# Kernel optimization log

Measured on AMD Instinct MI355X. Metric: run time of the kernel, lower is better.

Reference implementation:

```python
import jax, jax.numpy as jnp
import numpy as np

PROP_TIME = 8  # matches init_kwargs prop_time


def _patches(x, dil):
    # x: [B,1,H,W] -> [B,9,H,W]; 'same' padding with the given dilation,
    # matching torch.nn.functional.unfold(kernel_size=3, dilation=dil, padding=dil).
    return jax.lax.conv_general_dilated_patches(
        x,
        filter_shape=(3, 3),
        window_strides=(1, 1),
        padding=[(dil, dil), (dil, dil)],
        rhs_dilation=(dil, dil),
    )


def setup_inputs() -> dict:
    key = jax.random.key(0)
    k1, k2, k3, k4 = jax.random.split(key, 4)
    B, H, W = 4, 352, 1216
    guided1 = jax.random.normal(k1, (B, 9, H, W), dtype=jnp.float32)
    guided2 = jax.random.normal(k2, (B, 9, H, W), dtype=jnp.float32)
    fuse = jax.random.uniform(k3, (B, 2, H, W), dtype=jnp.float32)
    x = jax.random.normal(k4, (B, 1, H, W), dtype=jnp.float32)
    return {"guided1": guided1, "guided2": guided2, "fuse": fuse, "x": x}


def reference(guided1, guided2, fuse, x):
    # softmax over the 9 kernel taps -> spatially varying normalized kernels
    kern1 = jax.nn.softmax(guided1, axis=1)  # [B,9,H,W]
    kern2 = jax.nn.softmax(guided2, axis=1)  # [B,9,H,W]
    f1 = fuse[:, 0:1]  # [B,1,H,W]
    f2 = fuse[:, 1:2]
    for _ in range(PROP_TIME):
        p1 = _patches(x, 1)  # [B,9,H,W]
        p2 = _patches(x, 2)
        o1 = jnp.sum(p1 * kern1, axis=1, keepdims=True)  # [B,1,H,W]
        o2 = jnp.sum(p2 * kern2, axis=1, keepdims=True)
        x = o1 * f1 + o2 * f2
    return x
```

## Files before the change

kernel.cpp:

```cpp
#include <hip/hip_runtime.h>

#define HH 352
#define WW 1216
#define NB 4
#define HWSZ (HH * WW)
#define WQ 304
#define NQ (NB * HH * WQ)

typedef _Float16 half8 __attribute__((ext_vector_type(8)));


__global__ __launch_bounds__(256, 2) void softmax_premul_kernel(
    const float* __restrict__ g1, const float* __restrict__ g2,
    const float* __restrict__ fuse, _Float16* __restrict__ ko) {
    int q = blockIdx.x * 256 + threadIdx.x;
    if (q >= NQ) return;
    int b   = q / (HH * WQ);
    int rem = q - b * (HH * WQ);
    long gbase = (long)b * 9 * HWSZ + (long)rem * 4;
    long fbase = (long)b * 2 * HWSZ + (long)rem * 4;

    float4 t[18];
#pragma unroll
    for (int k = 0; k < 9; k++) t[k]     = *(const float4*)(g1 + gbase + (long)k * HWSZ);
#pragma unroll
    for (int k = 0; k < 9; k++) t[9 + k] = *(const float4*)(g2 + gbase + (long)k * HWSZ);
    float4 f1 = *(const float4*)(fuse + fbase);
    float4 f2 = *(const float4*)(fuse + fbase + HWSZ);

    float s1[4] = {0.f, 0.f, 0.f, 0.f}, s2[4] = {0.f, 0.f, 0.f, 0.f};
#pragma unroll
    for (int k = 0; k < 9; k++) {
        t[k].x = __expf(t[k].x); s1[0] += t[k].x;
        t[k].y = __expf(t[k].y); s1[1] += t[k].y;
        t[k].z = __expf(t[k].z); s1[2] += t[k].z;
        t[k].w = __expf(t[k].w); s1[3] += t[k].w;
    }
#pragma unroll
    for (int k = 9; k < 18; k++) {
        t[k].x = __expf(t[k].x); s2[0] += t[k].x;
        t[k].y = __expf(t[k].y); s2[1] += t[k].y;
        t[k].z = __expf(t[k].z); s2[2] += t[k].z;
        t[k].w = __expf(t[k].w); s2[3] += t[k].w;
    }
    float r1[4], r2[4];
    r1[0] = f1.x / s1[0]; r1[1] = f1.y / s1[1]; r1[2] = f1.z / s1[2]; r1[3] = f1.w / s1[3];
    r2[0] = f2.x / s2[0]; r2[1] = f2.y / s2[1]; r2[2] = f2.z / s2[2]; r2[3] = f2.w / s2[3];

    long obase = ((long)b * 9 * HWSZ + (long)rem * 4) * 2;
#pragma unroll
    for (int k = 0; k < 9; k++) {
        half8 o;
        o[0] = (_Float16)(t[k].x * r1[0]); o[1] = (_Float16)(t[9 + k].x * r2[0]);
        o[2] = (_Float16)(t[k].y * r1[1]); o[3] = (_Float16)(t[9 + k].y * r2[1]);
        o[4] = (_Float16)(t[k].z * r1[2]); o[5] = (_Float16)(t[9 + k].z * r2[2]);
        o[6] = (_Float16)(t[k].w * r1[3]); o[7] = (_Float16)(t[9 + k].w * r2[3]);
        *(half8*)(ko + obase + (long)k * HWSZ * 2) = o;
    }
}

#define CTH 8
#define CTQ 76
#define R1H 12
#define R1Q 78
#define X0H 16
#define X0Q 80
#define NREG (R1H * R1Q)

__global__ __launch_bounds__(512, 2) void prop2_kernel(
    const _Float16* __restrict__ kk,
    const float* __restrict__ xin, float* __restrict__ xout) {
    __shared__ float x0s[X0H][X0Q * 4];
    __shared__ float x1s[R1H][R1Q * 4];

    int tid  = threadIdx.x;
    int bidx = blockIdx.x;
    int tX = bidx & 3;
    int rr = bidx >> 2;
    int tY = rr % 44;
    int b  = rr / 44;
    int q0 = tX * CTQ;
    int h0 = tY * CTH;
    const float* xb = xin + (long)b * HWSZ;

    half8 kv[2][9];
    int own_r[2], own_c[2];
    bool own_v[2];
#pragma unroll
    for (int o = 0; o < 2; o++) {
        int idx = tid + o * 512;
        bool active = idx < NREG;
        int r = idx / R1Q;
        int c = idx - r * R1Q;
        own_r[o] = r; own_c[o] = c;
        int h  = h0 - 2 + r;
        int qg = q0 - 1 + c;
        bool valid = active && (h >= 0) && (h < HH) && (qg >= 0) && (qg < WQ);
        own_v[o] = active;
        long kb = ((long)b * 9 * HWSZ + (long)h * WW + qg * 4) * 2;
#pragma unroll
        for (int k = 0; k < 9; k++) {
            half8 z = {};
            kv[o][k] = valid ? *(const half8*)(kk + kb + (long)k * HWSZ * 2) : z;
        }
    }

    for (int i = tid; i < X0H * X0Q; i += 512) {
        int r = i / X0Q;
        int c = i - r * X0Q;
        int h  = h0 - 4 + r;
        int qg = q0 - 2 + c;
        float4 v = make_float4(0.f, 0.f, 0.f, 0.f);
        if (h >= 0 && h < HH && qg >= 0 && qg < WQ)
            v = *(const float4*)(xb + (long)h * WW + qg * 4);
        *(float4*)&x0s[r][c * 4] = v;
    }
    __syncthreads();

#pragma unroll
    for (int o = 0; o < 2; o++) {
        if (!own_v[o]) continue;
        int r = own_r[o], c = own_c[o];
        float rb[5][8];
#pragma unroll
        for (int y = 0; y < 5; y++) {
            const float* p = &x0s[r + y][4 * c + 2];
            float2 a = *(const float2*)(p);
            float4 m = *(const float4*)(p + 2);
            float2 z = *(const float2*)(p + 6);
            rb[y][0] = a.x; rb[y][1] = a.y;
            rb[y][2] = m.x; rb[y][3] = m.y; rb[y][4] = m.z; rb[y][5] = m.w;
            rb[y][6] = z.x; rb[y][7] = z.y;
        }
        float ov[4] = {0.f, 0.f, 0.f, 0.f};
#pragma unroll
        for (int ky = 0; ky < 3; ky++)
#pragma unroll
            for (int kx = 0; kx < 3; kx++) {
                int k = ky * 3 + kx;
#pragma unroll
                for (int j = 0; j < 4; j++) {
                    ov[j] = fmaf((float)kv[o][k][2 * j],     rb[ky + 1][j + 1 + kx], ov[j]);
                    ov[j] = fmaf((float)kv[o][k][2 * j + 1], rb[2 * ky][j + 2 * kx], ov[j]);
                }
            }
        *(float4*)&x1s[r][c * 4] = make_float4(ov[0], ov[1], ov[2], ov[3]);
    }
    __syncthreads();

#pragma unroll
    for (int o = 0; o < 2; o++) {
        int r = own_r[o], c = own_c[o];
        if (!own_v[o] || r < 2 || r >= 10 || c < 1 || c >= 77) continue;
        float rb[5][8];
#pragma unroll
        for (int y = 0; y < 5; y++) {
            const float* p = &x1s[r - 2 + y][4 * c - 2];
            float2 a = *(const float2*)(p);
            float4 m = *(const float4*)(p + 2);
            float2 z = *(const float2*)(p + 6);
            rb[y][0] = a.x; rb[y][1] = a.y;
            rb[y][2] = m.x; rb[y][3] = m.y; rb[y][4] = m.z; rb[y][5] = m.w;
            rb[y][6] = z.x; rb[y][7] = z.y;
        }
        float ov[4] = {0.f, 0.f, 0.f, 0.f};
#pragma unroll
        for (int ky = 0; ky < 3; ky++)
#pragma unroll
            for (int kx = 0; kx < 3; kx++) {
                int k = ky * 3 + kx;
#pragma unroll
                for (int j = 0; j < 4; j++) {
                    ov[j] = fmaf((float)kv[o][k][2 * j],     rb[ky + 1][j + 1 + kx], ov[j]);
                    ov[j] = fmaf((float)kv[o][k][2 * j + 1], rb[2 * ky][j + 2 * kx], ov[j]);
                }
            }
        int h  = h0 - 2 + r;
        int qg = q0 - 1 + c;
        *(float4*)(xout + (long)b * HWSZ + (long)h * WW + qg * 4) =
            make_float4(ov[0], ov[1], ov[2], ov[3]);
    }
}

extern "C" void kernel_launch(void* const* d_in, const int* in_sizes, int n_in,
                              void* d_out, int out_size, void* d_ws, size_t ws_size,
                              hipStream_t stream) {
    const float* g1   = (const float*)d_in[0];
    const float* g2   = (const float*)d_in[1];
    const float* fuse = (const float*)d_in[2];
    const float* x    = (const float*)d_in[3];
    float* out = (float*)d_out;

    _Float16* kk = (_Float16*)d_ws;
    float* bufA  = (float*)(kk + (size_t)NB * 9 * HWSZ * 2);

    int sm_blocks = (NQ + 255) / 256;
    softmax_premul_kernel<<<sm_blocks, 256, 0, stream>>>(g1, g2, fuse, kk);

    int pr_blocks = NB * 44 * 4;
    prop2_kernel<<<pr_blocks, 512, 0, stream>>>(kk, x,    bufA);
    prop2_kernel<<<pr_blocks, 512, 0, stream>>>(kk, bufA, out);
    prop2_kernel<<<pr_blocks, 512, 0, stream>>>(kk, out,  bufA);
    prop2_kernel<<<pr_blocks, 512, 0, stream>>>(kk, bufA, out);
}
```

Before: 276.9 us.

## Replace two-step shared-memory fused propagation with one-step-per-launch register stencil

Drops the LDS-tiled kernel that fused two propagation steps per launch (with halo recompute and block syncs). Adds a simple per-thread kernel that computes 8 outputs of one step straight from global memory, launched eight times. This removes the halo overhead and barriers, but the fp16 kernel tensor and x are now re-read every step instead of every two steps.

```diff
diff --git a/kernel.cpp b/kernel.cpp
--- a/kernel.cpp
+++ b/kernel.cpp
@@ -6,6 +6,8 @@
 #define HWSZ (HH * WW)
 #define WQ 304
 #define NQ (NB * HH * WQ)
+#define PPR 152
+#define NP (NB * HH * PPR)
 
 typedef _Float16 half8 __attribute__((ext_vector_type(8)));
 
@@ -59,127 +61,74 @@
     }
 }
 
-#define CTH 8
-#define CTQ 76
-#define R1H 12
-#define R1Q 78
-#define X0H 16
-#define X0Q 80
-#define NREG (R1H * R1Q)
-
-__global__ __launch_bounds__(512, 2) void prop2_kernel(
+__global__ __launch_bounds__(256, 2) void prop8_kernel(
     const _Float16* __restrict__ kk,
     const float* __restrict__ xin, float* __restrict__ xout) {
-    __shared__ float x0s[X0H][X0Q * 4];
-    __shared__ float x1s[R1H][R1Q * 4];
+    int p = blockIdx.x * 256 + threadIdx.x;
+    int b   = p / (HH * PPR);
+    int rem = p - b * (HH * PPR);
+    int h   = rem / PPR;
+    int pq  = rem - h * PPR;
+    int w0  = pq * 8;
 
-    int tid  = threadIdx.x;
-    int bidx = blockIdx.x;
-    int tX = bidx & 3;
-    int rr = bidx >> 2;
-    int tY = rr % 44;
-    int b  = rr / 44;
-    int q0 = tX * CTQ;
-    int h0 = tY * CTH;
     const float* xb = xin + (long)b * HWSZ;
+    long kbase = ((long)b * 9 * HWSZ + (long)h * WW + w0) * 2;
 
-    half8 kv[2][9];
-    int own_r[2], own_c[2];
-    bool own_v[2];
+    half8 kv[18];
 #pragma unroll
-    for (int o = 0; o < 2; o++) {
-        int idx = tid + o * 512;
-        bool active = idx < NREG;
-        int r = idx / R1Q;
-        int c = idx - r * R1Q;
-        own_r[o] = r; own_c[o] = c;
-        int h  = h0 - 2 + r;
-        int qg = q0 - 1 + c;
-        bool valid = active && (h >= 0) && (h < HH) && (qg >= 0) && (qg < WQ);
-        own_v[o] = active;
-        long kb = ((long)b * 9 * HWSZ + (long)h * WW + qg * 4) * 2;
+    for (int k = 0; k < 9; k++) {
+        kv[2 * k]     = *(const half8*)(kk + kbase + (long)k * HWSZ * 2);
+        kv[2 * k + 1] = *(const half8*)(kk + kbase + (long)k * HWSZ * 2 + 8);
+    }
+
+    float ml = (w0 > 0) ? 1.f : 0.f;
+    float mr = (w0 + 8 < WW) ? 1.f : 0.f;
+    int c0 = (w0 > 0) ? (w0 - 4) : 0;
+    int c3 = (w0 + 8 < WW) ? (w0 + 8) : (WW - 4);
+
+    float xf[5][16];
 #pragma unroll
-        for (int k = 0; k < 9; k++) {
-            half8 z = {};
-            kv[o][k] = valid ? *(const half8*)(kk + kb + (long)k * HWSZ * 2) : z;
+    for (int r = 0; r < 5; r++) {
+        int hh = h - 2 + r;
+        int hc = hh < 0 ? 0 : (hh >= HH ? HH - 1 : hh);
+        float mv = (hh >= 0 && hh < HH) ? 1.f : 0.f;
+        const float* rp = xb + (long)hc * WW;
+        float4 v0 = *(const float4*)(rp + c0);
+        float4 v1 = *(const float4*)(rp + w0);
+        float4 v2 = *(const float4*)(rp + w0 + 4);
+        float4 v3 = *(const float4*)(rp + c3);
+        float mlv = mv * ml, mrv = mv * mr;
+        xf[r][0]  = v0.x * mlv; xf[r][1]  = v0.y * mlv;
+        xf[r][2]  = v0.z * mlv; xf[r][3]  = v0.w * mlv;
+        xf[r][4]  = v1.x * mv;  xf[r][5]  = v1.y * mv;
+        xf[r][6]  = v1.z * mv;  xf[r][7]  = v1.w * mv;
+        xf[r][8]  = v2.x * mv;  xf[r][9]  = v2.y * mv;
+        xf[r][10] = v2.z * mv;  xf[r][11] = v2.w * mv;
+        xf[r][12] = v3.x * mrv; xf[r][13] = v3.y * mrv;
+        xf[r][14] = v3.z * mrv; xf[r][15] = v3.w * mrv;
+    }
+
+    float o[8] = {0.f, 0.f, 0.f, 0.f, 0.f, 0.f, 0.f, 0.f};
+#pragma unroll
+    for (int ky = 0; ky < 3; ky++) {
+#pragma unroll
+        for (int kx = 0; kx < 3; kx++) {
+            int k = ky * 3 + kx;
+#pragma unroll
+            for (int qd = 0; qd < 2; qd++) {
+#pragma unroll
+                for (int jj = 0; jj < 4; jj++) {
+                    int j = 4 * qd + jj;
+                    o[j] = fmaf((float)kv[2 * k + qd][2 * jj],     xf[ky + 1][j + 3 + kx],     o[j]);
+                    o[j] = fmaf((float)kv[2 * k + qd][2 * jj + 1], xf[2 * ky][j + 2 + 2 * kx], o[j]);
+                }
+            }
         }
     }
 
-    for (int i = tid; i < X0H * X0Q; i += 512) {
-        int r = i / X0Q;
-        int c = i - r * X0Q;
-        int h  = h0 - 4 + r;
-        int qg = q0 - 2 + c;
-        float4 v = make_float4(0.f, 0.f, 0.f, 0.f);
-        if (h >= 0 && h < HH && qg >= 0 && qg < WQ)
-            v = *(const float4*)(xb + (long)h * WW + qg * 4);
-        *(float4*)&x0s[r][c * 4] = v;
-    }
-    __syncthreads();
-
-#pragma unroll
-    for (int o = 0; o < 2; o++) {
-        if (!own_v[o]) continue;
-        int r = own_r[o], c = own_c[o];
-        float rb[5][8];
-#pragma unroll
-        for (int y = 0; y < 5; y++) {
-            const float* p = &x0s[r + y][4 * c + 2];
-            float2 a = *(const float2*)(p);
-            float4 m = *(const float4*)(p + 2);
-            float2 z = *(const float2*)(p + 6);
-            rb[y][0] = a.x; rb[y][1] = a.y;
-            rb[y][2] = m.x; rb[y][3] = m.y; rb[y][4] = m.z; rb[y][5] = m.w;
-            rb[y][6] = z.x; rb[y][7] = z.y;
-        }
-        float ov[4] = {0.f, 0.f, 0.f, 0.f};
-#pragma unroll
-        for (int ky = 0; ky < 3; ky++)
-#pragma unroll
-            for (int kx = 0; kx < 3; kx++) {
-                int k = ky * 3 + kx;
-#pragma unroll
-                for (int j = 0; j < 4; j++) {
-                    ov[j] = fmaf((float)kv[o][k][2 * j],     rb[ky + 1][j + 1 + kx], ov[j]);
-                    ov[j] = fmaf((float)kv[o][k][2 * j + 1], rb[2 * ky][j + 2 * kx], ov[j]);
-                }
-            }
-        *(float4*)&x1s[r][c * 4] = make_float4(ov[0], ov[1], ov[2], ov[3]);
-    }
-    __syncthreads();
-
-#pragma unroll
-    for (int o = 0; o < 2; o++) {
-        int r = own_r[o], c = own_c[o];
-        if (!own_v[o] || r < 2 || r >= 10 || c < 1 || c >= 77) continue;
-        float rb[5][8];
-#pragma unroll
-        for (int y = 0; y < 5; y++) {
-            const float* p = &x1s[r - 2 + y][4 * c - 2];
-            float2 a = *(const float2*)(p);
-            float4 m = *(const float4*)(p + 2);
-            float2 z = *(const float2*)(p + 6);
-            rb[y][0] = a.x; rb[y][1] = a.y;
-            rb[y][2] = m.x; rb[y][3] = m.y; rb[y][4] = m.z; rb[y][5] = m.w;
-            rb[y][6] = z.x; rb[y][7] = z.y;
-        }
-        float ov[4] = {0.f, 0.f, 0.f, 0.f};
-#pragma unroll
-        for (int ky = 0; ky < 3; ky++)
-#pragma unroll
-            for (int kx = 0; kx < 3; kx++) {
-                int k = ky * 3 + kx;
-#pragma unroll
-                for (int j = 0; j < 4; j++) {
-                    ov[j] = fmaf((float)kv[o][k][2 * j],     rb[ky + 1][j + 1 + kx], ov[j]);
-                    ov[j] = fmaf((float)kv[o][k][2 * j + 1], rb[2 * ky][j + 2 * kx], ov[j]);
-                }
-            }
-        int h  = h0 - 2 + r;
-        int qg = q0 - 1 + c;
-        *(float4*)(xout + (long)b * HWSZ + (long)h * WW + qg * 4) =
-            make_float4(ov[0], ov[1], ov[2], ov[3]);
-    }
+    float* op = xout + (long)b * HWSZ + (long)h * WW + w0;
+    *(float4*)op       = make_float4(o[0], o[1], o[2], o[3]);
+    *(float4*)(op + 4) = make_float4(o[4], o[5], o[6], o[7]);
 }
 
 extern "C" void kernel_launch(void* const* d_in, const int* in_sizes, int n_in,
@@ -197,9 +146,13 @@
     int sm_blocks = (NQ + 255) / 256;
     softmax_premul_kernel<<<sm_blocks, 256, 0, stream>>>(g1, g2, fuse, kk);
 
-    int pr_blocks = NB * 44 * 4;
-    prop2_kernel<<<pr_blocks, 512, 0, stream>>>(kk, x,    bufA);
-    prop2_kernel<<<pr_blocks, 512, 0, stream>>>(kk, bufA, out);
-    prop2_kernel<<<pr_blocks, 512, 0, stream>>>(kk, out,  bufA);
-    prop2_kernel<<<pr_blocks, 512, 0, stream>>>(kk, bufA, out);
+    int pr_blocks = NP / 256;
+    prop8_kernel<<<pr_blocks, 256, 0, stream>>>(kk, x,    bufA);
+    prop8_kernel<<<pr_blocks, 256, 0, stream>>>(kk, bufA, out);
+    prop8_kernel<<<pr_blocks, 256, 0, stream>>>(kk, out,  bufA);
+    prop8_kernel<<<pr_blocks, 256, 0, stream>>>(kk, bufA, out);
+    prop8_kernel<<<pr_blocks, 256, 0, stream>>>(kk, out,  bufA);
+    prop8_kernel<<<pr_blocks, 256, 0, stream>>>(kk, bufA, out);
+    prop8_kernel<<<pr_blocks, 256, 0, stream>>>(kk, out,  bufA);
+    prop8_kernel<<<pr_blocks, 256, 0, stream>>>(kk, bufA, out);
 }
```

After: 333.3 us. 20.4% more time.
